# Kernel tuning notes

Measured on AMD Instinct MI355X. Metric: run time of the kernel, lower is better.

## Reference

```python
import jax, jax.numpy as jnp
import numpy as np

N = 50000     # nodes
E = 800000    # edges (avg degree 16)
DIN = 128     # in_size
DH = 256      # hidden_size
P = 100000    # pos/neg edge pairs


def _w(key, fan_in, shape):
    return jax.random.normal(key, shape, jnp.float32) * (1.0 / np.sqrt(fan_in))


def setup_inputs() -> dict:
    key = jax.random.key(0)
    ks = jax.random.split(key, 24)
    inp = {}
    inp['x'] = jax.random.normal(ks[0], (N, DIN), jnp.float32)
    inp['edge_src'] = jax.random.randint(ks[1], (E,), 0, N, dtype=jnp.int32)
    inp['edge_dst'] = jax.random.randint(ks[2], (E,), 0, N, dtype=jnp.int32)
    inp['pos_src'] = jax.random.randint(ks[3], (P,), 0, N, dtype=jnp.int32)
    inp['pos_dst'] = jax.random.randint(ks[4], (P,), 0, N, dtype=jnp.int32)
    inp['neg_src'] = jax.random.randint(ks[5], (P,), 0, N, dtype=jnp.int32)
    inp['neg_dst'] = jax.random.randint(ks[6], (P,), 0, N, dtype=jnp.int32)
    # SAGEConv layers: fc_self + fc_neigh + bias
    dims = [(DIN, DH), (DH, DH), (DH, DH)]
    for i, (di, do) in enumerate(dims):
        inp[f'Ws{i}'] = _w(ks[7 + 3 * i], di, (di, do))
        inp[f'Wn{i}'] = _w(ks[8 + 3 * i], di, (di, do))
        inp[f'b{i}'] = jnp.zeros((do,), jnp.float32)
    # predictor MLP: DH -> DH -> DH -> 1
    inp['Wp1'] = _w(ks[16], DH, (DH, DH)); inp['bp1'] = jnp.zeros((DH,), jnp.float32)
    inp['Wp2'] = _w(ks[17], DH, (DH, DH)); inp['bp2'] = jnp.zeros((DH,), jnp.float32)
    inp['Wp3'] = _w(ks[18], DH, (DH, 1)); inp['bp3'] = jnp.zeros((1,), jnp.float32)
    return inp


def _sage_layer(h, src, dst, Ws, Wn, b):
    # mean aggregation over incoming edges, then fc_self(h) + fc_neigh(agg) + b
    n = h.shape[0]
    msg = h[src]                                              # [E, d] gather
    deg = jax.ops.segment_sum(jnp.ones((src.shape[0],), h.dtype), dst, num_segments=n)
    agg = jax.ops.segment_sum(msg, dst, num_segments=n)
    agg = agg / jnp.maximum(deg, 1.0)[:, None]
    return h @ Ws + agg @ Wn + b


def reference(x, edge_src, edge_dst, pos_src, pos_dst, neg_src, neg_dst,
              Ws0, Wn0, b0, Ws1, Wn1, b1, Ws2, Wn2, b2,
              Wp1, bp1, Wp2, bp2, Wp3, bp3):
    h = x
    layers = [(Ws0, Wn0, b0), (Ws1, Wn1, b1), (Ws2, Wn2, b2)]
    for i, (Ws, Wn, bb) in enumerate(layers):
        h = _sage_layer(h, edge_src, edge_dst, Ws, Wn, bb)
        if i < len(layers) - 1:
            h = jax.nn.relu(h)

    def predictor(e):
        z = jax.nn.relu(e @ Wp1 + bp1)
        z = jax.nn.relu(z @ Wp2 + bp2)
        return z @ Wp3 + bp3

    hidden_pos = predictor(h[pos_src] * h[pos_dst])   # [P, 1]
    hidden_neg = predictor(h[neg_src] * h[neg_dst])   # [P, 1]
    return (hidden_pos, hidden_neg)
```

## Files before the change

### kernel.cpp

```cpp
#include <hip/hip_runtime.h>
#include <hip/hip_bf16.h>

#define CDIV(a, b) (((a) + (b) - 1) / (b))

typedef __attribute__((ext_vector_type(8))) __bf16 bf16x8;
typedef __attribute__((ext_vector_type(2))) __bf16 bf16x2;
typedef __attribute__((ext_vector_type(4))) float f32x4;

__device__ __forceinline__ float bf2f(unsigned short u) {
  union { unsigned int i; float f; } c; c.i = ((unsigned int)u) << 16; return c.f;
}
__device__ __forceinline__ unsigned short f2bf(float f) {
  union { float f; unsigned int i; } c; c.f = f;
  unsigned int r = c.i + 0x7fffu + ((c.i >> 16) & 1u);
  return (unsigned short)(r >> 16);
}
__device__ __forceinline__ unsigned int cvt2(float a, float b) {
  bf16x2 v; v[0] = (__bf16)a; v[1] = (__bf16)b;
  union { bf16x2 v; unsigned int u; } c; c.v = v; return c.u;
}
__device__ __forceinline__ unsigned short cvt1(float a) {
  __bf16 b = (__bf16)a;
  union { __bf16 b; unsigned short u; } c; c.b = b; return c.u;
}

__global__ void k_detect(const unsigned short* __restrict__ xq, int nsamp, int* __restrict__ flagp) {
  __shared__ float sm[256];
  int t = threadIdx.x;
  float mx = 0.f;
  for (int i = t; i < nsamp; i += 256) {
    float v = bf2f(xq[i]);
    if (!(v == v)) v = 1e30f;
    mx = fmaxf(mx, fabsf(v));
  }
  sm[t] = mx; __syncthreads();
  for (int o = 128; o > 0; o >>= 1) {
    if (t < o) sm[t] = fmaxf(sm[t], sm[t + o]);
    __syncthreads();
  }
  if (t == 0) *flagp = (sm[0] > 1e6f) ? 1 : 0;
}

__global__ void k_cvt7(const void* p0, const void* p1, const void* p2, const void* p3,
                       const void* p4, const void* p5, const void* p6,
                       float* d0, float* d1, float* d2, float* d3,
                       float* d4, float* d5, float* d6, const int* __restrict__ flagp) {
  int b = blockIdx.x, t = threadIdx.x;
  const void* s = 0; float* d = 0; int n = 256;
  switch (b) {
    case 0: s = p0; d = d0; break;
    case 1: s = p1; d = d1; break;
    case 2: s = p2; d = d2; break;
    case 3: s = p3; d = d3; break;
    case 4: s = p4; d = d4; break;
    case 5: s = p5; d = d5; break;
    default: s = p6; d = d6; n = 1; break;
  }
  if (t < n) d[t] = (*flagp) ? ((const float*)s)[t] : bf2f(((const unsigned short*)s)[t]);
}

__global__ void k_wh8(const void* s0, const void* s1, const void* s2, const void* s3,
                      const void* s4, const void* s5, const void* s6, const void* s7,
                      unsigned short* d0, unsigned short* d1, unsigned short* d2,
                      unsigned short* d3, unsigned short* d4, unsigned short* d5,
                      unsigned short* d6, unsigned short* d7,
                      const int* __restrict__ flagp) {
  int b = blockIdx.x;
  const void* W; unsigned short* Bt; int K; int base;
  if (b < 128)       { W = s0; Bt = d0; K = 128; base = 0; }
  else if (b < 256)  { W = s1; Bt = d1; K = 128; base = 128; }
  else {
    int r = (b - 256) >> 8;
    base = 256 + r * 256; K = 256;
    switch (r) {
      case 0:  W = s2; Bt = d2; break;
      case 1:  W = s3; Bt = d3; break;
      case 2:  W = s4; Bt = d4; break;
      case 3:  W = s5; Bt = d5; break;
      case 4:  W = s6; Bt = d6; break;
      default: W = s7; Bt = d7; break;
    }
  }
  int i = (b - base) * 256 + threadIdx.x;
  int k = i >> 8, n = i & 255;
  float v = (*flagp) ? ((const float*)W)[i] : bf2f(((const unsigned short*)W)[i]);
  Bt[(size_t)n * K + k] = f2bf(v);
}

__global__ void k_xbf16(const void* __restrict__ x, unsigned short* __restrict__ Xb, int n,
                        const int* __restrict__ flagp) {
  int i = blockIdx.x * 256 + threadIdx.x;
  if (i >= n) return;
  float v = (*flagp) ? ((const float*)x)[i] : bf2f(((const unsigned short*)x)[i]);
  Xb[i] = f2bf(v);
}

__global__ void k_zero_i32(int* p, int n) {
  int i = blockIdx.x * 256 + threadIdx.x;
  if (i < n) p[i] = 0;
}

__global__ void k_deg(const int* __restrict__ dst, int* __restrict__ deg, int E) {
  int e = blockIdx.x * 256 + threadIdx.x;
  if (e < E) atomicAdd(&deg[dst[e]], 1);
}
__global__ void k_scan1(const int* __restrict__ in, int* __restrict__ out, int* __restrict__ bsums, int n) {
  __shared__ int sh[256];
  int t = threadIdx.x, i = blockIdx.x * 256 + t;
  int v = (i < n) ? in[i] : 0;
  sh[t] = v; __syncthreads();
  for (int o = 1; o < 256; o <<= 1) {
    int add = (t >= o) ? sh[t - o] : 0;
    __syncthreads();
    sh[t] += add;
    __syncthreads();
  }
  if (i < n) out[i] = sh[t] - v;
  if (t == 255) bsums[blockIdx.x] = sh[255];
}
__global__ void k_scan2(int* bsums, int nb) {
  __shared__ int sh[256];
  int t = threadIdx.x;
  int v = (t < nb) ? bsums[t] : 0;
  sh[t] = v; __syncthreads();
  for (int o = 1; o < 256; o <<= 1) {
    int add = (t >= o) ? sh[t - o] : 0;
    __syncthreads();
    sh[t] += add;
    __syncthreads();
  }
  if (t < nb) bsums[t] = sh[t] - v;
}
__global__ void k_scan3(int* offs, const int* bsums, int n, int etot) {
  int i = blockIdx.x * 256 + threadIdx.x;
  if (i < n) offs[i] += bsums[blockIdx.x];
  if (i == 0) offs[n] = etot;
}
__global__ void k_copy_i32(const int* __restrict__ a, int* __restrict__ b, int n) {
  int i = blockIdx.x * 256 + threadIdx.x;
  if (i < n) b[i] = a[i];
}
__global__ void k_fill(const int* __restrict__ dst, const int* __restrict__ src,
                       int* __restrict__ cursor, int* __restrict__ csr_src, int E) {
  int e = blockIdx.x * 256 + threadIdx.x;
  if (e >= E) return;
  int pos = atomicAdd(&cursor[dst[e]], 1);
  csr_src[pos] = src[e];
}
__global__ void k_sortw(const int* __restrict__ offs, int* __restrict__ csr, int n) {
  int w = threadIdx.x >> 6, lane = threadIdx.x & 63;
  int v = blockIdx.x * 4 + w;
  if (v >= n) return;
  int s = offs[v], e = offs[v + 1];
  int deg = e - s;
  if (deg <= 1) return;
  if (deg > 64) {
    if (lane == 0) {
      for (int i = s + 1; i < e; ++i) {
        int key = csr[i], j = i - 1;
        while (j >= s && csr[j] > key) { csr[j + 1] = csr[j]; --j; }
        csr[j + 1] = key;
      }
    }
    return;
  }
  int val = (lane < deg) ? csr[s + lane] : 0x7fffffff;
#pragma unroll
  for (int k = 2; k <= 64; k <<= 1) {
    bool dir = (lane & k) == 0;
#pragma unroll
    for (int j = k >> 1; j > 0; j >>= 1) {
      int p = __shfl_xor(val, j, 64);
      bool lower = (lane & j) == 0;
      val = (lower == dir) ? min(val, p) : max(val, p);
    }
  }
  if (lane < deg) csr[s + lane] = val;
}

#define ACC8(V)                                              \
  do {                                                       \
    a0 += bf2f((unsigned short)(V).x);                       \
    a1 += bf2f((unsigned short)((V).x >> 16));               \
    a2 += bf2f((unsigned short)(V).y);                       \
    a3 += bf2f((unsigned short)((V).y >> 16));               \
    a4 += bf2f((unsigned short)(V).z);                       \
    a5 += bf2f((unsigned short)((V).z >> 16));               \
    a6 += bf2f((unsigned short)(V).w);                       \
    a7 += bf2f((unsigned short)((V).w >> 16));               \
  } while (0)

__global__ void k_agg(const unsigned short* __restrict__ H, int Kd,
                      const int* __restrict__ offs, const int* __restrict__ csr,
                      unsigned short* __restrict__ Ab) {
  int w = threadIdx.x >> 6, lane = threadIdx.x & 63;
  int v = blockIdx.x * 4 + w;
  int s = offs[v], e = offs[v + 1];
  float inv = 1.f / fmaxf((float)(e - s), 1.f);
  float a0 = 0.f, a1 = 0.f, a2 = 0.f, a3 = 0.f;
  float a4 = 0.f, a5 = 0.f, a6 = 0.f, a7 = 0.f;
  if (Kd == 256) {
    int half = lane >> 5;
    int li = lane & 31;
    int c8 = li * 8;
    int i = s;
    for (; i + 8 <= e; i += 8) {
      uint4 q0 = *(const uint4*)&H[(size_t)csr[i     + half] * 256 + c8];
      uint4 q1 = *(const uint4*)&H[(size_t)csr[i + 2 + half] * 256 + c8];
      uint4 q2 = *(const uint4*)&H[(size_t)csr[i + 4 + half] * 256 + c8];
      uint4 q3 = *(const uint4*)&H[(size_t)csr[i + 6 + half] * 256 + c8];
      ACC8(q0); ACC8(q1); ACC8(q2); ACC8(q3);
    }
    for (; i + 2 <= e; i += 2) {
      uint4 q0 = *(const uint4*)&H[(size_t)csr[i + half] * 256 + c8];
      ACC8(q0);
    }
    if (i < e && half == 0) {
      uint4 q0 = *(const uint4*)&H[(size_t)csr[i] * 256 + c8];
      ACC8(q0);
    }
    a0 += __shfl_xor(a0, 32, 64); a1 += __shfl_xor(a1, 32, 64);
    a2 += __shfl_xor(a2, 32, 64); a3 += __shfl_xor(a3, 32, 64);
    a4 += __shfl_xor(a4, 32, 64); a5 += __shfl_xor(a5, 32, 64);
    a6 += __shfl_xor(a6, 32, 64); a7 += __shfl_xor(a7, 32, 64);
    if (half == 0) {
      uint4 o;
      o.x = cvt2(a0 * inv, a1 * inv);
      o.y = cvt2(a2 * inv, a3 * inv);
      o.z = cvt2(a4 * inv, a5 * inv);
      o.w = cvt2(a6 * inv, a7 * inv);
      *(uint4*)&Ab[(size_t)v * 256 + c8] = o;
    }
  } else {
    int hf = lane >> 4;
    int li = lane & 15;
    int c8 = li * 8;
    int i = s;
    for (; i + 16 <= e; i += 16) {
      uint4 q0 = *(const uint4*)&H[(size_t)csr[i      + hf] * 128 + c8];
      uint4 q1 = *(const uint4*)&H[(size_t)csr[i + 4  + hf] * 128 + c8];
      uint4 q2 = *(const uint4*)&H[(size_t)csr[i + 8  + hf] * 128 + c8];
      uint4 q3 = *(const uint4*)&H[(size_t)csr[i + 12 + hf] * 128 + c8];
      ACC8(q0); ACC8(q1); ACC8(q2); ACC8(q3);
    }
    for (; i + 4 <= e; i += 4) {
      uint4 q0 = *(const uint4*)&H[(size_t)csr[i + hf] * 128 + c8];
      ACC8(q0);
    }
    if (hf < e - i) {
      uint4 q0 = *(const uint4*)&H[(size_t)csr[i + hf] * 128 + c8];
      ACC8(q0);
    }
    a0 += __shfl_xor(a0, 16, 64); a1 += __shfl_xor(a1, 16, 64);
    a2 += __shfl_xor(a2, 16, 64); a3 += __shfl_xor(a3, 16, 64);
    a4 += __shfl_xor(a4, 16, 64); a5 += __shfl_xor(a5, 16, 64);
    a6 += __shfl_xor(a6, 16, 64); a7 += __shfl_xor(a7, 16, 64);
    a0 += __shfl_xor(a0, 32, 64); a1 += __shfl_xor(a1, 32, 64);
    a2 += __shfl_xor(a2, 32, 64); a3 += __shfl_xor(a3, 32, 64);
    a4 += __shfl_xor(a4, 32, 64); a5 += __shfl_xor(a5, 32, 64);
    a6 += __shfl_xor(a6, 32, 64); a7 += __shfl_xor(a7, 32, 64);
    if (lane < 16) {
      uint4 o;
      o.x = cvt2(a0 * inv, a1 * inv);
      o.y = cvt2(a2 * inv, a3 * inv);
      o.z = cvt2(a4 * inv, a5 * inv);
      o.w = cvt2(a6 * inv, a7 * inv);
      *(uint4*)&Ab[(size_t)v * 128 + c8] = o;
    }
  }
}

__global__ __launch_bounds__(256) void gemm_cat(
    const unsigned short* __restrict__ A1, const unsigned short* __restrict__ A2, int K,
    const unsigned short* __restrict__ B1h, const unsigned short* __restrict__ B2h,
    const float* __restrict__ bias, int relu, int M, unsigned short* __restrict__ O) {
  __shared__ unsigned short sAh[128 * 40], sBh[128 * 40];
  int t = threadIdx.x;
  int mt = blockIdx.x >> 1, nt = blockIdx.x & 1;
  int m0 = mt * 128;
  int n0 = nt * 128;
  int wid = t >> 6, lane = t & 63;
  int wr = (wid >> 1) * 64, wc = (wid & 1) * 64;
  int quad = lane >> 4, lrow = lane & 15;

  f32x4 acc[4][4];
  const f32x4 z4 = {0.f, 0.f, 0.f, 0.f};
#pragma unroll
  for (int i = 0; i < 4; ++i)
#pragma unroll
    for (int j = 0; j < 4; ++j) acc[i][j] = z4;

  int sr = t >> 2;
  int c8 = (t & 3) * 8;
  int ar0 = m0 + sr;      if (ar0 >= M) ar0 = M - 1;
  int ar1 = m0 + sr + 64; if (ar1 >= M) ar1 = M - 1;
  int br0 = n0 + sr, br1 = n0 + sr + 64;

  int kc = K >> 5;
  int nsteps = kc * 2;

  uint4 pfA0 = *(const uint4*)&A1[(size_t)ar0 * K + c8];
  uint4 pfA1 = *(const uint4*)&A1[(size_t)ar1 * K + c8];
  uint4 pfB0 = *(const uint4*)&B1h[(size_t)br0 * K + c8];
  uint4 pfB1 = *(const uint4*)&B1h[(size_t)br1 * K + c8];

  for (int s2 = 0; s2 < nsteps; ++s2) {
    *(uint4*)&sAh[sr * 40 + c8] = pfA0;
    *(uint4*)&sAh[(sr + 64) * 40 + c8] = pfA1;
    *(uint4*)&sBh[sr * 40 + c8] = pfB0;
    *(uint4*)&sBh[(sr + 64) * 40 + c8] = pfB1;
    int s1 = s2 + 1;
    if (s1 < nsteps) {
      const unsigned short* Ap = (s1 >= kc) ? A2 : A1;
      const unsigned short* Bp = (s1 >= kc) ? B2h : B1h;
      int k0 = ((s1 >= kc) ? (s1 - kc) : s1) * 32;
      pfA0 = *(const uint4*)&Ap[(size_t)ar0 * K + k0 + c8];
      pfA1 = *(const uint4*)&Ap[(size_t)ar1 * K + k0 + c8];
      pfB0 = *(const uint4*)&Bp[(size_t)br0 * K + k0 + c8];
      pfB1 = *(const uint4*)&Bp[(size_t)br1 * K + k0 + c8];
    }
    __syncthreads();
    bf16x8 ah[4], bh[4];
#pragma unroll
    for (int i = 0; i < 4; ++i) {
      ah[i] = *(const bf16x8*)&sAh[(wr + i * 16 + lrow) * 40 + quad * 8];
      bh[i] = *(const bf16x8*)&sBh[(wc + i * 16 + lrow) * 40 + quad * 8];
    }
#pragma unroll
    for (int i = 0; i < 4; ++i)
#pragma unroll
      for (int j = 0; j < 4; ++j)
        acc[i][j] = __builtin_amdgcn_mfma_f32_16x16x32_bf16(ah[i], bh[j], acc[i][j], 0, 0, 0);
    __syncthreads();
  }

#pragma unroll
  for (int j = 0; j < 4; ++j) {
    int gc = n0 + wc + j * 16 + lrow;
    float bv = bias[gc];
#pragma unroll
    for (int i = 0; i < 4; ++i) {
#pragma unroll
      for (int rr = 0; rr < 4; ++rr) {
        int gr = m0 + wr + i * 16 + quad * 4 + rr;
        if (gr < M) {
          float v = acc[i][j][rr] + bv;
          if (relu) v = fmaxf(v, 0.f);
          O[(size_t)gr * 256 + gc] = cvt1(v);
        }
      }
    }
  }
}

__global__ __launch_bounds__(256, 3) void gemm_pred_fused(
    const unsigned short* __restrict__ Hb,
    const int* __restrict__ ps, const int* __restrict__ pd,
    const int* __restrict__ ns, const int* __restrict__ nd,
    int nPos,
    const unsigned short* __restrict__ B1h, const float* __restrict__ bp1c,
    const unsigned short* __restrict__ B2h, const float* __restrict__ bp2c,
    const float* __restrict__ wp3, const float* __restrict__ bp3c,
    void* __restrict__ out, const int* __restrict__ flagp) {
  __shared__ __align__(16) unsigned short zT[64 * 264];
  __shared__ __align__(16) unsigned short sBh[256 * 40];
  int t = threadIdx.x;
  int m0 = blockIdx.x * 64;
  int wid = t >> 6, lane = t & 63;
  int wc = wid * 64;
  int quad = lane >> 4, lrow = lane & 15;

  int sr = t >> 2;
  int c8 = (t & 3) * 8;
  int c64 = (t & 3) * 64;

  int arow = m0 + sr;
  int s, d;
  if (arow < nPos) { s = ps[arow]; d = pd[arow]; }
  else             { s = ns[arow - nPos]; d = nd[arow - nPos]; }
  const unsigned short* Hs = &Hb[(size_t)s * 256];
  const unsigned short* Hd = &Hb[(size_t)d * 256];

#pragma unroll
  for (int u = 0; u < 8; ++u) {
    uint4 hs = *(const uint4*)(Hs + c64 + u * 8);
    uint4 hd = *(const uint4*)(Hd + c64 + u * 8);
    uint4 o;
    o.x = cvt2(bf2f((unsigned short)hs.x) * bf2f((unsigned short)hd.x),
               bf2f((unsigned short)(hs.x >> 16)) * bf2f((unsigned short)(hd.x >> 16)));
    o.y = cvt2(bf2f((unsigned short)hs.y) * bf2f((unsigned short)hd.y),
               bf2f((unsigned short)(hs.y >> 16)) * bf2f((unsigned short)(hd.y >> 16)));
    o.z = cvt2(bf2f((unsigned short)hs.z) * bf2f((unsigned short)hd.z),
               bf2f((unsigned short)(hs.z >> 16)) * bf2f((unsigned short)(hd.z >> 16)));
    o.w = cvt2(bf2f((unsigned short)hs.w) * bf2f((unsigned short)hd.w),
               bf2f((unsigned short)(hs.w >> 16)) * bf2f((unsigned short)(hd.w >> 16)));
    *(uint4*)&zT[sr * 264 + c64 + u * 8] = o;
  }

  f32x4 acc[4][4];
  const f32x4 z4 = {0.f, 0.f, 0.f, 0.f};
#pragma unroll
  for (int i = 0; i < 4; ++i)
#pragma unroll
    for (int j = 0; j < 4; ++j) acc[i][j] = z4;

  for (int k0 = 0; k0 < 256; k0 += 32) {
#pragma unroll
    for (int rep = 0; rep < 4; ++rep) {
      int r = sr + rep * 64;
      *(uint4*)&sBh[r * 40 + c8] = *(const uint4*)&B1h[(size_t)r * 256 + k0 + c8];
    }
    __syncthreads();
    bf16x8 ah[4], bh[4];
#pragma unroll
    for (int i = 0; i < 4; ++i) {
      ah[i] = *(const bf16x8*)&zT[(i * 16 + lrow) * 264 + k0 + quad * 8];
      bh[i] = *(const bf16x8*)&sBh[(wc + i * 16 + lrow) * 40 + quad * 8];
    }
#pragma unroll
    for (int i = 0; i < 4; ++i)
#pragma unroll
      for (int j = 0; j < 4; ++j)
        acc[i][j] = __builtin_amdgcn_mfma_f32_16x16x32_bf16(ah[i], bh[j], acc[i][j], 0, 0, 0);
    __syncthreads();
  }

#pragma unroll
  for (int j = 0; j < 4; ++j) {
    int gc = wc + j * 16 + lrow;
    float bv = bp1c[gc];
#pragma unroll
    for (int i = 0; i < 4; ++i) {
#pragma unroll
      for (int rr = 0; rr < 4; ++rr) {
        int rloc = i * 16 + quad * 4 + rr;
        float v = fmaxf(acc[i][j][rr] + bv, 0.f);
        zT[rloc * 264 + gc] = cvt1(v);
      }
    }
  }

#pragma unroll
  for (int i = 0; i < 4; ++i)
#pragma unroll
    for (int j = 0; j < 4; ++j) acc[i][j] = z4;

  for (int k0 = 0; k0 < 256; k0 += 32) {
#pragma unroll
    for (int rep = 0; rep < 4; ++rep) {
      int r = sr + rep * 64;
      *(uint4*)&sBh[r * 40 + c8] = *(const uint4*)&B2h[(size_t)r * 256 + k0 + c8];
    }
    __syncthreads();
    bf16x8 ah[4], bh[4];
#pragma unroll
    for (int i = 0; i < 4; ++i) {
      ah[i] = *(const bf16x8*)&zT[(i * 16 + lrow) * 264 + k0 + quad * 8];
      bh[i] = *(const bf16x8*)&sBh[(wc + i * 16 + lrow) * 40 + quad * 8];
    }
#pragma unroll
    for (int i = 0; i < 4; ++i)
#pragma unroll
      for (int j = 0; j < 4; ++j)
        acc[i][j] = __builtin_amdgcn_mfma_f32_16x16x32_bf16(ah[i], bh[j], acc[i][j], 0, 0, 0);
    __syncthreads();
  }

  float* part = (float*)sBh;
  int cid = wid * 16 + lrow;
#pragma unroll
  for (int i = 0; i < 4; ++i) {
#pragma unroll
    for (int rr = 0; rr < 4; ++rr) {
      int rloc = i * 16 + quad * 4 + rr;
      float sum = 0.f;
#pragma unroll
      for (int j = 0; j < 4; ++j) {
        int gc = wc + j * 16 + lrow;
        float v = fmaxf(acc[i][j][rr] + bp2c[gc], 0.f);
        sum += v * wp3[gc];
      }
      part[rloc * 65 + cid] = sum;
    }
  }
  __syncthreads();
  if (t < 64) {
    int gr = m0 + t;
    float ssum = 0.f;
#pragma unroll
    for (int c = 0; c < 64; ++c) ssum += part[t * 65 + c];
    ssum += bp3c[0];
    if (*flagp) ((float*)out)[gr] = ssum;
    else        ((unsigned short*)out)[gr] = f2bf(ssum);
  }
}

extern "C" void kernel_launch(void* const* d_in, const int* in_sizes, int n_in,
                              void* d_out, int out_size, void* d_ws, size_t ws_size,
                              hipStream_t stream) {
  const int N = 50000, E = 800000, P = 100000, DIN = 128, DH = 256;
  const int M2 = 2 * P;
  const void* x = d_in[0];
  const int* esrc = (const int*)d_in[1];
  const int* edst = (const int*)d_in[2];
  const int* psrc = (const int*)d_in[3];
  const int* pdst = (const int*)d_in[4];
  const int* nsrc = (const int*)d_in[5];
  const int* ndst = (const int*)d_in[6];
  const void* Ws0 = d_in[7];  const void* Wn0 = d_in[8];  const void* b0 = d_in[9];
  const void* Ws1 = d_in[10]; const void* Wn1 = d_in[11]; const void* b1 = d_in[12];
  const void* Ws2 = d_in[13]; const void* Wn2 = d_in[14]; const void* b2 = d_in[15];
  const void* Wp1 = d_in[16]; const void* bp1 = d_in[17];
  const void* Wp2 = d_in[18]; const void* bp2 = d_in[19];
  const void* Wp3 = d_in[20]; const void* bp3 = d_in[21];
  (void)in_sizes; (void)n_in; (void)out_size; (void)ws_size;

  const size_t NH = (size_t)N * DH;
  unsigned short* planeA = (unsigned short*)d_ws;
  unsigned short* Xb = planeA;
  char* reg1 = (char*)d_ws + NH * 2;
  unsigned short* AggB  = (unsigned short*)reg1;
  unsigned short* planeB = (unsigned short*)(reg1 + NH * 4);
  float* P0 = (float*)(reg1 + (size_t)M2 * 256 * 2);
  float* P1 = P0 + M2;
  unsigned short* W16 = (unsigned short*)(P1 + M2);
  unsigned short* ws0h = W16;
  unsigned short* wn0h = ws0h + 32768;
  unsigned short* ws1h = wn0h + 32768;
  unsigned short* wn1h = ws1h + 65536;
  unsigned short* ws2h = wn1h + 65536;
  unsigned short* wn2h = ws2h + 65536;
  unsigned short* wp1h = wn2h + 65536;
  unsigned short* wp2h = wp1h + 65536;
  float* FB = (float*)(wp2h + 65536);
  float* b0f  = FB;
  float* b1f  = b0f + 256;
  float* b2f  = b1f + 256;
  float* bp1f = b2f + 256;
  float* bp2f = bp1f + 256;
  float* wp3f = bp2f + 256;
  float* bp3f = wp3f + 256;
  int* deg   = (int*)(bp3f + 4);
  int* offs  = deg + N;
  int* cur   = offs + (N + 1);
  int* bsums = cur + N;
  int* csr   = bsums + 256;
  int* flagp = csr + E;

  k_detect<<<1, 256, 0, stream>>>((const unsigned short*)x, 8192, flagp);

  k_wh8<<<1792, 256, 0, stream>>>(Ws0, Wn0, Ws1, Wn1, Ws2, Wn2, Wp1, Wp2,
                                  ws0h, wn0h, ws1h, wn1h, ws2h, wn2h, wp1h, wp2h,
                                  flagp);
  k_cvt7<<<7, 256, 0, stream>>>(b0, b1, b2, bp1, bp2, Wp3, bp3,
                                b0f, b1f, b2f, bp1f, bp2f, wp3f, bp3f, flagp);

  int nb = CDIV(N, 256);
  k_zero_i32<<<nb, 256, 0, stream>>>(deg, N);
  k_deg<<<CDIV(E, 256), 256, 0, stream>>>(edst, deg, E);
  k_scan1<<<nb, 256, 0, stream>>>(deg, offs, bsums, N);
  k_scan2<<<1, 256, 0, stream>>>(bsums, nb);
  k_scan3<<<nb, 256, 0, stream>>>(offs, bsums, N, E);
  k_copy_i32<<<nb, 256, 0, stream>>>(offs, cur, N);
  k_fill<<<CDIV(E, 256), 256, 0, stream>>>(edst, esrc, cur, csr, E);
  k_sortw<<<CDIV(N, 4), 256, 0, stream>>>(offs, csr, N);

  const int G_L = CDIV(N, 128) * 2;

  k_xbf16<<<CDIV(N * DIN, 256), 256, 0, stream>>>(x, Xb, N * DIN, flagp);
  k_agg<<<N / 4, 256, 0, stream>>>(Xb, DIN, offs, csr, AggB);
  gemm_cat<<<G_L, 256, 0, stream>>>(Xb, AggB, DIN, ws0h, wn0h, b0f, 1, N, planeB);

  k_agg<<<N / 4, 256, 0, stream>>>(planeB, DH, offs, csr, AggB);
  gemm_cat<<<G_L, 256, 0, stream>>>(planeB, AggB, DH, ws1h, wn1h, b1f, 1, N, planeA);

  k_agg<<<N / 4, 256, 0, stream>>>(planeA, DH, offs, csr, AggB);
  gemm_cat<<<G_L, 256, 0, stream>>>(planeA, AggB, DH, ws2h, wn2h, b2f, 0, N, planeB);

  gemm_pred_fused<<<M2 / 64, 256, 0, stream>>>(planeB, psrc, pdst, nsrc, ndst, P,
                                               wp1h, bp1f, wp2h, bp2f, wp3f, bp3f,
                                               d_out, flagp);
}
```

Before: 612.6 us.

## Widen SAGE GEMM tile to full 256 columns and merge small setup kernels

The SAGE layer GEMM now uses 512-thread blocks that each compute a 128x256 output tile. Each A row tile is loaded once instead of by two blocks, which halves A global traffic and the block count. Separately, the bias conversion kernel is folded into the weight transpose kernel, and the cursor copy is folded into the final scan pass, removing two launches. The larger block needs more shared memory per block and may lower occupancy.

Result: faster. 575.8 us (-6.0%).

```diff
diff --git a/kernel.cpp b/kernel.cpp
--- a/kernel.cpp
+++ b/kernel.cpp
@@ -41,31 +41,32 @@
   if (t == 0) *flagp = (sm[0] > 1e6f) ? 1 : 0;
 }
 
-__global__ void k_cvt7(const void* p0, const void* p1, const void* p2, const void* p3,
-                       const void* p4, const void* p5, const void* p6,
-                       float* d0, float* d1, float* d2, float* d3,
-                       float* d4, float* d5, float* d6, const int* __restrict__ flagp) {
-  int b = blockIdx.x, t = threadIdx.x;
-  const void* s = 0; float* d = 0; int n = 256;
-  switch (b) {
-    case 0: s = p0; d = d0; break;
-    case 1: s = p1; d = d1; break;
-    case 2: s = p2; d = d2; break;
-    case 3: s = p3; d = d3; break;
-    case 4: s = p4; d = d4; break;
-    case 5: s = p5; d = d5; break;
-    default: s = p6; d = d6; n = 1; break;
-  }
-  if (t < n) d[t] = (*flagp) ? ((const float*)s)[t] : bf2f(((const unsigned short*)s)[t]);
-}
-
 __global__ void k_wh8(const void* s0, const void* s1, const void* s2, const void* s3,
                       const void* s4, const void* s5, const void* s6, const void* s7,
                       unsigned short* d0, unsigned short* d1, unsigned short* d2,
                       unsigned short* d3, unsigned short* d4, unsigned short* d5,
                       unsigned short* d6, unsigned short* d7,
+                      const void* p0, const void* p1, const void* p2, const void* p3,
+                      const void* p4, const void* p5, const void* p6,
+                      float* f0, float* f1, float* f2, float* f3,
+                      float* f4, float* f5, float* f6,
                       const int* __restrict__ flagp) {
-  int b = blockIdx.x;
+  int b = blockIdx.x, t = threadIdx.x;
+  if (b >= 1792) {
+    int c = b - 1792;
+    const void* s = 0; float* d = 0; int n = 256;
+    switch (c) {
+      case 0: s = p0; d = f0; break;
+      case 1: s = p1; d = f1; break;
+      case 2: s = p2; d = f2; break;
+      case 3: s = p3; d = f3; break;
+      case 4: s = p4; d = f4; break;
+      case 5: s = p5; d = f5; break;
+      default: s = p6; d = f6; n = 1; break;
+    }
+    if (t < n) d[t] = (*flagp) ? ((const float*)s)[t] : bf2f(((const unsigned short*)s)[t]);
+    return;
+  }
   const void* W; unsigned short* Bt; int K; int base;
   if (b < 128)       { W = s0; Bt = d0; K = 128; base = 0; }
   else if (b < 256)  { W = s1; Bt = d1; K = 128; base = 128; }
@@ -81,7 +82,7 @@
       default: W = s7; Bt = d7; break;
     }
   }
-  int i = (b - base) * 256 + threadIdx.x;
+  int i = (b - base) * 256 + t;
   int k = i >> 8, n = i & 255;
   float v = (*flagp) ? ((const float*)W)[i] : bf2f(((const unsigned short*)W)[i]);
   Bt[(size_t)n * K + k] = f2bf(v);
@@ -131,14 +132,14 @@
   }
   if (t < nb) bsums[t] = sh[t] - v;
 }
-__global__ void k_scan3(int* offs, const int* bsums, int n, int etot) {
+__global__ void k_scan3(int* offs, int* cur, const int* bsums, int n, int etot) {
   int i = blockIdx.x * 256 + threadIdx.x;
-  if (i < n) offs[i] += bsums[blockIdx.x];
+  if (i < n) {
+    int o = offs[i] + bsums[blockIdx.x];
+    offs[i] = o;
+    cur[i] = o;
+  }
   if (i == 0) offs[n] = etot;
-}
-__global__ void k_copy_i32(const int* __restrict__ a, int* __restrict__ b, int n) {
-  int i = blockIdx.x * 256 + threadIdx.x;
-  if (i < n) b[i] = a[i];
 }
 __global__ void k_fill(const int* __restrict__ dst, const int* __restrict__ src,
                        int* __restrict__ cursor, int* __restrict__ csr_src, int E) {
@@ -270,17 +271,17 @@
   }
 }
 
-__global__ __launch_bounds__(256) void gemm_cat(
+__global__ __launch_bounds__(512) void gemm_cat(
     const unsigned short* __restrict__ A1, const unsigned short* __restrict__ A2, int K,
     const unsigned short* __restrict__ B1h, const unsigned short* __restrict__ B2h,
     const float* __restrict__ bias, int relu, int M, unsigned short* __restrict__ O) {
-  __shared__ unsigned short sAh[128 * 40], sBh[128 * 40];
+  __shared__ unsigned short sAh[128 * 40];
+  __shared__ unsigned short sBh[256 * 40];
   int t = threadIdx.x;
-  int mt = blockIdx.x >> 1, nt = blockIdx.x & 1;
-  int m0 = mt * 128;
-  int n0 = nt * 128;
+  int m0 = blockIdx.x * 128;
   int wid = t >> 6, lane = t & 63;
-  int wr = (wid >> 1) * 64, wc = (wid & 1) * 64;
+  int wr = (wid >> 2) * 64;
+  int wc = (wid & 3) * 64;
   int quad = lane >> 4, lrow = lane & 15;
 
   f32x4 acc[4][4];
@@ -290,34 +291,31 @@
 #pragma unroll
     for (int j = 0; j < 4; ++j) acc[i][j] = z4;
 
-  int sr = t >> 2;
-  int c8 = (t & 3) * 8;
-  int ar0 = m0 + sr;      if (ar0 >= M) ar0 = M - 1;
-  int ar1 = m0 + sr + 64; if (ar1 >= M) ar1 = M - 1;
-  int br0 = n0 + sr, br1 = n0 + sr + 64;
+  int sra = t >> 2;
+  int c8a = (t & 3) * 8;
+  int ar = m0 + sra; if (ar >= M) ar = M - 1;
+  int brow0 = t >> 2,         bc0 = (t & 3) * 8;
+  int brow1 = 128 + (t >> 2), bc1 = bc0;
 
   int kc = K >> 5;
   int nsteps = kc * 2;
 
-  uint4 pfA0 = *(const uint4*)&A1[(size_t)ar0 * K + c8];
-  uint4 pfA1 = *(const uint4*)&A1[(size_t)ar1 * K + c8];
-  uint4 pfB0 = *(const uint4*)&B1h[(size_t)br0 * K + c8];
-  uint4 pfB1 = *(const uint4*)&B1h[(size_t)br1 * K + c8];
+  uint4 pfA  = *(const uint4*)&A1[(size_t)ar * K + c8a];
+  uint4 pfB0 = *(const uint4*)&B1h[(size_t)brow0 * K + bc0];
+  uint4 pfB1 = *(const uint4*)&B1h[(size_t)brow1 * K + bc1];
 
   for (int s2 = 0; s2 < nsteps; ++s2) {
-    *(uint4*)&sAh[sr * 40 + c8] = pfA0;
-    *(uint4*)&sAh[(sr + 64) * 40 + c8] = pfA1;
-    *(uint4*)&sBh[sr * 40 + c8] = pfB0;
-    *(uint4*)&sBh[(sr + 64) * 40 + c8] = pfB1;
+    *(uint4*)&sAh[sra * 40 + c8a] = pfA;
+    *(uint4*)&sBh[brow0 * 40 + bc0] = pfB0;
+    *(uint4*)&sBh[brow1 * 40 + bc1] = pfB1;
     int s1 = s2 + 1;
     if (s1 < nsteps) {
       const unsigned short* Ap = (s1 >= kc) ? A2 : A1;
       const unsigned short* Bp = (s1 >= kc) ? B2h : B1h;
       int k0 = ((s1 >= kc) ? (s1 - kc) : s1) * 32;
-      pfA0 = *(const uint4*)&Ap[(size_t)ar0 * K + k0 + c8];
-      pfA1 = *(const uint4*)&Ap[(size_t)ar1 * K + k0 + c8];
-      pfB0 = *(const uint4*)&Bp[(size_t)br0 * K + k0 + c8];
-      pfB1 = *(const uint4*)&Bp[(size_t)br1 * K + k0 + c8];
+      pfA  = *(const uint4*)&Ap[(size_t)ar * K + k0 + c8a];
+      pfB0 = *(const uint4*)&Bp[(size_t)brow0 * K + k0 + bc0];
+      pfB1 = *(const uint4*)&Bp[(size_t)brow1 * K + k0 + bc1];
     }
     __syncthreads();
     bf16x8 ah[4], bh[4];
@@ -336,7 +334,7 @@
 
 #pragma unroll
   for (int j = 0; j < 4; ++j) {
-    int gc = n0 + wc + j * 16 + lrow;
+    int gc = wc + j * 16 + lrow;
     float bv = bias[gc];
 #pragma unroll
     for (int i = 0; i < 4; ++i) {
@@ -549,33 +547,32 @@
 
   k_detect<<<1, 256, 0, stream>>>((const unsigned short*)x, 8192, flagp);
 
-  k_wh8<<<1792, 256, 0, stream>>>(Ws0, Wn0, Ws1, Wn1, Ws2, Wn2, Wp1, Wp2,
+  k_wh8<<<1799, 256, 0, stream>>>(Ws0, Wn0, Ws1, Wn1, Ws2, Wn2, Wp1, Wp2,
                                   ws0h, wn0h, ws1h, wn1h, ws2h, wn2h, wp1h, wp2h,
+                                  b0, b1, b2, bp1, bp2, Wp3, bp3,
+                                  b0f, b1f, b2f, bp1f, bp2f, wp3f, bp3f,
                                   flagp);
-  k_cvt7<<<7, 256, 0, stream>>>(b0, b1, b2, bp1, bp2, Wp3, bp3,
-                                b0f, b1f, b2f, bp1f, bp2f, wp3f, bp3f, flagp);
 
   int nb = CDIV(N, 256);
   k_zero_i32<<<nb, 256, 0, stream>>>(deg, N);
   k_deg<<<CDIV(E, 256), 256, 0, stream>>>(edst, deg, E);
   k_scan1<<<nb, 256, 0, stream>>>(deg, offs, bsums, N);
   k_scan2<<<1, 256, 0, stream>>>(bsums, nb);
-  k_scan3<<<nb, 256, 0, stream>>>(offs, bsums, N, E);
-  k_copy_i32<<<nb, 256, 0, stream>>>(offs, cur, N);
+  k_scan3<<<nb, 256, 0, stream>>>(offs, cur, bsums, N, E);
   k_fill<<<CDIV(E, 256), 256, 0, stream>>>(edst, esrc, cur, csr, E);
   k_sortw<<<CDIV(N, 4), 256, 0, stream>>>(offs, csr, N);
 
-  const int G_L = CDIV(N, 128) * 2;
+  const int G_C = CDIV(N, 128);
 
   k_xbf16<<<CDIV(N * DIN, 256), 256, 0, stream>>>(x, Xb, N * DIN, flagp);
   k_agg<<<N / 4, 256, 0, stream>>>(Xb, DIN, offs, csr, AggB);
-  gemm_cat<<<G_L, 256, 0, stream>>>(Xb, AggB, DIN, ws0h, wn0h, b0f, 1, N, planeB);
+  gemm_cat<<<G_C, 512, 0, stream>>>(Xb, AggB, DIN, ws0h, wn0h, b0f, 1, N, planeB);
 
   k_agg<<<N / 4, 256, 0, stream>>>(planeB, DH, offs, csr, AggB);
-  gemm_cat<<<G_L, 256, 0, stream>>>(planeB, AggB, DH, ws1h, wn1h, b1f, 1, N, planeA);
+  gemm_cat<<<G_C, 512, 0, stream>>>(planeB, AggB, DH, ws1h, wn1h, b1f, 1, N, planeA);
 
   k_agg<<<N / 4, 256, 0, stream>>>(planeA, DH, offs, csr, AggB);
-  gemm_cat<<<G_L, 256, 0, stream>>>(planeA, AggB, DH, ws2h, wn2h, b2f, 0, N, planeB);
+  gemm_cat<<<G_C, 512, 0, stream>>>(planeA, AggB, DH, ws2h, wn2h, b2f, 0, N, planeB);
 
   gemm_pred_fused<<<M2 / 64, 256, 0, stream>>>(planeB, psrc, pdst, nsrc, ndst, P,
                                                wp1h, bp1f, wp2h, bp2f, wp3f, bp3f,
```
